# Performance work log

Measured on AMD Instinct MI355X. Metric: run time of the kernel, lower is better.

Reference implementation:

```python
import jax, jax.numpy as jnp
import numpy as np

D_MODEL = 1024
NUM_HEADS = 16
HEAD_DIM = D_MODEL // NUM_HEADS


def setup_inputs() -> dict:
    key = jax.random.key(0)
    ks = jax.random.split(key, 5)
    B, S = 2, 2048
    x = jax.random.normal(ks[0], (B, S, D_MODEL), dtype=jnp.float32)
    # nn.Linear(d,d,bias=False): y = x @ W.T, W is [out,in]. Init ~ U(-1/sqrt(d), 1/sqrt(d)).
    lim = 1.0 / np.sqrt(D_MODEL)
    wq = jax.random.uniform(ks[1], (D_MODEL, D_MODEL), jnp.float32, -lim, lim)
    wk = jax.random.uniform(ks[2], (D_MODEL, D_MODEL), jnp.float32, -lim, lim)
    wv = jax.random.uniform(ks[3], (D_MODEL, D_MODEL), jnp.float32, -lim, lim)
    wo = jax.random.uniform(ks[4], (D_MODEL, D_MODEL), jnp.float32, -lim, lim)
    return {"x": x, "wq": wq, "wk": wk, "wv": wv, "wo": wo}


def reference(x, wq, wk, wv, wo):
    B, S, D = x.shape
    H, Hd = NUM_HEADS, HEAD_DIM
    scale = Hd ** 0.5
    # projections (torch Linear: x @ W.T), split heads -> [B,H,S,Hd]
    q = (x @ wq.T).reshape(B, S, H, Hd).transpose(0, 2, 1, 3)
    k = (x @ wk.T).reshape(B, S, H, Hd).transpose(0, 2, 1, 3)
    v = (x @ wv.T).reshape(B, S, H, Hd).transpose(0, 2, 1, 3)
    scores = jnp.einsum('bhqd,bhkd->bhqk', q, k) / scale  # [B,H,S,S]
    # causal mask: disallow j > i
    causal_mask = jnp.triu(jnp.ones((S, S), dtype=bool), k=1)
    scores = jnp.where(causal_mask, -jnp.inf, scores)
    attn = jax.nn.softmax(scores, axis=-1)
    out = jnp.einsum('bhqk,bhkd->bhqd', attn, v)
    out = out.transpose(0, 2, 1, 3).reshape(B, S, D)
    return out @ wo.T
```

## Files before the change

kernel.cpp:

```cpp
#include <hip/hip_runtime.h>

#define DEV __device__ __forceinline__

typedef __attribute__((ext_vector_type(4))) float f32x4;
typedef __attribute__((ext_vector_type(8))) __bf16 bf16x8;

typedef __attribute__((address_space(1))) const uint32_t gu32;
typedef __attribute__((address_space(3))) uint32_t su32;

DEV void gload16(const void* g, void* s) {
  __builtin_amdgcn_global_load_lds((gu32*)(uintptr_t)g,
                                   (su32*)(uint32_t)(uintptr_t)s, 16, 0, 0);
}

DEV ushort bfbits(float f) { return __builtin_bit_cast(ushort, (__bf16)f); }

DEV bf16x8 lds8(const ushort* p) {
  return __builtin_bit_cast(bf16x8, *(const uint4*)(p));
}

DEV void vmcnt0bar() {
  asm volatile("s_waitcnt vmcnt(0)" ::: "memory");
  __builtin_amdgcn_s_barrier();
}

__global__ void cvt_all(const float* __restrict__ x, const float* __restrict__ wq,
                        const float* __restrict__ wk, const float* __restrict__ wv,
                        const float* __restrict__ wo, ushort* __restrict__ xb,
                        ushort* __restrict__ wb) {
  int i = blockIdx.x * blockDim.x + threadIdx.x;
  const float* src; ushort* dst; float scl = 1.0f; int j;
  if (i < 1048576) { src = x; dst = xb; j = i; }
  else {
    int t = (i - 1048576) >> 18;
    j = (i - 1048576) & 262143;
    src = t == 0 ? wq : (t == 1 ? wk : (t == 2 ? wv : wo));
    dst = wb + t * 1048576;
    if (t == 0) scl = 0.18033688011f;
  }
  float4 v = ((const float4*)src)[j];
  ushort4 o;
  o.x = bfbits(v.x * scl); o.y = bfbits(v.y * scl);
  o.z = bfbits(v.z * scl); o.w = bfbits(v.w * scl);
  ((ushort4*)dst)[j] = o;
}

template <int NFR, int OUT_MODE>
DEV void gemm_core(const ushort* __restrict__ A, const ushort* __restrict__ W,
                   void* __restrict__ Cout, ushort* sA, ushort* sB) {
  const int tid = threadIdx.x;
  const int l = tid & 63, wv = tid >> 6;
  const int g = l >> 4, lan = l & 15;
  const int wr = wv >> 1, wc = wv & 1;
  const int brow = blockIdx.y * 128, bcol = blockIdx.x * (NFR * 32);
  const int ASZ = 128 * 32, BSZ = NFR * 32 * 32;

  f32x4 acc[4][NFR] = {};

  auto stage = [&](int buf, int k0) {
    ushort* dA = sA + buf * ASZ;
    ushort* dB = sB + buf * BSZ;
#pragma unroll
    for (int i = 0; i < 2; ++i) {
      int n = i * 256 + wv * 64 + l;
      int row = n >> 2, ss = n & 3, gs = (ss - (row >> 1)) & 3;
      gload16(A + (size_t)(brow + row) * 1024 + k0 + gs * 8,
              dA + (i * 256 + wv * 64) * 8);
    }
#pragma unroll
    for (int i = 0; i < NFR / 2; ++i) {
      int n = i * 256 + wv * 64 + l;
      int row = n >> 2, ss = n & 3, gs = (ss - (row >> 1)) & 3;
      gload16(W + (size_t)(bcol + row) * 1024 + k0 + gs * 8,
              dB + (i * 256 + wv * 64) * 8);
    }
  };

  auto compute = [&](int buf) {
    const ushort* cA = sA + buf * ASZ;
    const ushort* cB = sB + buf * BSZ;
    bf16x8 a[4], b[NFR];
#pragma unroll
    for (int fr = 0; fr < 4; ++fr) {
      int row = wr * 64 + fr * 16 + lan;
      a[fr] = lds8(cA + row * 32 + 8 * (((row >> 1) + g) & 3));
    }
#pragma unroll
    for (int fn = 0; fn < NFR; ++fn) {
      int row = wc * (NFR * 16) + fn * 16 + lan;
      b[fn] = lds8(cB + row * 32 + 8 * (((row >> 1) + g) & 3));
    }
    __builtin_amdgcn_s_setprio(1);
#pragma unroll
    for (int fr = 0; fr < 4; ++fr)
#pragma unroll
      for (int fn = 0; fn < NFR; ++fn)
        acc[fr][fn] = __builtin_amdgcn_mfma_f32_16x16x32_bf16(a[fr], b[fn], acc[fr][fn], 0, 0, 0);
    __builtin_amdgcn_s_setprio(0);
  };

  stage(0, 0);
  vmcnt0bar();
#pragma unroll 1
  for (int t = 0; t < 15; ++t) {
    stage(1, (2 * t + 1) * 32); compute(0); vmcnt0bar();
    stage(0, (2 * t + 2) * 32); compute(1); vmcnt0bar();
  }
  stage(1, 31 * 32); compute(0); vmcnt0bar();
  compute(1);

#pragma unroll
  for (int fr = 0; fr < 4; ++fr)
#pragma unroll
    for (int fn = 0; fn < NFR; ++fn) {
      if (OUT_MODE == 2) {
        int row = brow + wr * 64 + fr * 16 + g * 4;
        int col = bcol + wc * (NFR * 16) + fn * 16 + lan;
        int bh2 = (row >> 11) * 16 + (col >> 6);
        int d = col & 63, s0 = row & 2047;
        ushort4 pk;
        pk.x = bfbits(acc[fr][fn][0]); pk.y = bfbits(acc[fr][fn][1]);
        pk.z = bfbits(acc[fr][fn][2]); pk.w = bfbits(acc[fr][fn][3]);
        *(ushort4*)((ushort*)Cout + ((size_t)bh2 * 64 + d) * 2048 + s0) = pk;
      } else {
#pragma unroll
        for (int r = 0; r < 4; ++r) {
          int row = brow + wr * 64 + fr * 16 + g * 4 + r;
          int col = bcol + wc * (NFR * 16) + fn * 16 + lan;
          if (OUT_MODE == 1)
            ((float*)Cout)[(size_t)row * 1024 + col] = acc[fr][fn][r];
          else
            ((ushort*)Cout)[(size_t)row * 1024 + col] = bfbits(acc[fr][fn][r]);
        }
      }
    }
}

__global__ __launch_bounds__(256) void gemm_qkv(
    const ushort* __restrict__ X, const ushort* __restrict__ Wb,
    ushort* __restrict__ Q, ushort* __restrict__ K, ushort* __restrict__ Vt) {
  __shared__ __align__(16) ushort sA[2 * 128 * 32];
  __shared__ __align__(16) ushort sB[2 * 128 * 32];
  const ushort* W = Wb + (size_t)blockIdx.z * 1048576;
  if (blockIdx.z == 2)
    gemm_core<4, 2>(X, W, (void*)Vt, sA, sB);
  else
    gemm_core<4, 0>(X, W, (void*)(blockIdx.z == 0 ? Q : K), sA, sB);
}

__global__ __launch_bounds__(256) void gemm_out(
    const ushort* __restrict__ AO, const ushort* __restrict__ Wo, float* __restrict__ C) {
  __shared__ __align__(16) ushort sA[2 * 128 * 32];
  __shared__ __align__(16) ushort sB[2 * 64 * 32];
  gemm_core<2, 1>(AO, Wo, (void*)C, sA, sB);
}

__global__ __launch_bounds__(256) void attn_fwd(
    const ushort* __restrict__ Qm, const ushort* __restrict__ Km,
    const ushort* __restrict__ Vtm, ushort* __restrict__ AO) {
  __shared__ __align__(16) ushort sK[2][64 * 64];
  __shared__ __align__(16) ushort sV[2][64 * 64];
  __shared__ __align__(16) ushort sP[4 * 16 * 64];

  const int tid = threadIdx.x;
  const int l = tid & 63, wv = tid >> 6;
  const int g = l >> 4, lan = l & 15;
  const int bid = blockIdx.x;
  const int j = bid >> 8, c = bid & 255;
  const int u = c >> 3, vv = c & 7;
  const int w = (u + ((j >> 1) << 4)) & 31;
  const int qt = (j & 1) ? (31 - w) : w;
  const int bh = vv + 8 * j;
  const int b = bh >> 4, h = bh & 15;
  const int q0 = qt * 64 + wv * 16;
  const int qg = q0 + lan;

  bf16x8 qf[2];
#pragma unroll
  for (int kf = 0; kf < 2; ++kf)
    qf[kf] = __builtin_bit_cast(bf16x8,
        *(const uint4*)(Qm + (size_t)(b * 2048 + qg) * 1024 + h * 64 + kf * 32 + g * 8));

  float lrun = 0.f;
  f32x4 o[4];
#pragma unroll
  for (int of = 0; of < 4; ++of) o[of] = (f32x4){0.f, 0.f, 0.f, 0.f};

  ushort* Pw = sP + wv * 1024;
  const int nkt = qt + 1;

  auto stagekv = [&](int buf, int kt) {
#pragma unroll
    for (int i = 0; i < 2; ++i) {
      int n = i * 256 + wv * 64 + l;
      int row = n >> 3, ss = n & 7, gs = ss ^ (row & 7);
      gload16(Km + (size_t)(b * 2048 + kt * 64 + row) * 1024 + h * 64 + gs * 8,
              sK[buf] + (i * 256 + wv * 64) * 8);
      gload16(Vtm + ((size_t)bh * 64 + row) * 2048 + kt * 64 + gs * 8,
              sV[buf] + (i * 256 + wv * 64) * 8);
    }
  };

  stagekv(0, 0);
  vmcnt0bar();

#pragma unroll 1
  for (int kt = 0; kt < nkt; ++kt) {
    const int buf = kt & 1;
    if (kt + 1 < nkt) stagekv(buf ^ 1, kt + 1);

    f32x4 sc[4];
    __builtin_amdgcn_s_setprio(1);
#pragma unroll
    for (int kvf = 0; kvf < 4; ++kvf) {
      f32x4 a2 = (f32x4){0.f, 0.f, 0.f, 0.f};
#pragma unroll
      for (int kf = 0; kf < 2; ++kf) {
        int row = kvf * 16 + lan;
        bf16x8 kb = lds8(sK[buf] + row * 64 + 8 * ((kf * 4 + g) ^ (row & 7)));
        a2 = __builtin_amdgcn_mfma_f32_16x16x32_bf16(kb, qf[kf], a2, 0, 0, 0);
      }
      sc[kvf] = a2;
    }
    __builtin_amdgcn_s_setprio(0);

    if (kt == qt) {
#pragma unroll
      for (int kvf = 0; kvf < 4; ++kvf)
#pragma unroll
        for (int r = 0; r < 4; ++r) {
          int kvg = kt * 64 + kvf * 16 + 4 * g + r;
          float p = __builtin_exp2f(sc[kvf][r]);
          p = (kvg <= qg) ? p : 0.f;
          sc[kvf][r] = p;
          lrun += p;
        }
    } else {
#pragma unroll
      for (int kvf = 0; kvf < 4; ++kvf)
#pragma unroll
        for (int r = 0; r < 4; ++r) {
          float p = __builtin_exp2f(sc[kvf][r]);
          sc[kvf][r] = p;
          lrun += p;
        }
    }

#pragma unroll
    for (int kvf = 0; kvf < 4; ++kvf) {
      ushort4 pk;
      pk.x = bfbits(sc[kvf][0]); pk.y = bfbits(sc[kvf][1]);
      pk.z = bfbits(sc[kvf][2]); pk.w = bfbits(sc[kvf][3]);
      *(ushort4*)(Pw + lan * 64 + ((16 * kvf + 4 * g) ^ ((lan & 7) << 3))) = pk;
    }
    bf16x8 pa[2];
#pragma unroll
    for (int kf = 0; kf < 2; ++kf)
      pa[kf] = lds8(Pw + lan * 64 + ((32 * kf + 8 * g) ^ ((lan & 7) << 3)));

    __builtin_amdgcn_s_setprio(1);
#pragma unroll
    for (int of = 0; of < 4; ++of)
#pragma unroll
      for (int kf = 0; kf < 2; ++kf) {
        int row = of * 16 + lan;
        bf16x8 vb = lds8(sV[buf] + row * 64 + 8 * ((kf * 4 + g) ^ (row & 7)));
        o[of] = __builtin_amdgcn_mfma_f32_16x16x32_bf16(pa[kf], vb, o[of], 0, 0, 0);
      }
    __builtin_amdgcn_s_setprio(0);

    vmcnt0bar();
  }

  lrun += __shfl_xor(lrun, 16);
  lrun += __shfl_xor(lrun, 32);
#pragma unroll
  for (int r = 0; r < 4; ++r) {
    float il = 1.0f / __shfl(lrun, g * 4 + r);
#pragma unroll
    for (int of = 0; of < 4; ++of) {
      int grow = q0 + g * 4 + r;
      AO[(size_t)(b * 2048 + grow) * 1024 + h * 64 + of * 16 + lan] = bfbits(o[of][r] * il);
    }
  }
}

extern "C" void kernel_launch(void* const* d_in, const int* in_sizes, int n_in,
                              void* d_out, int out_size, void* d_ws, size_t ws_size,
                              hipStream_t stream) {
  const float* x  = (const float*)d_in[0];
  const float* wq = (const float*)d_in[1];
  const float* wk = (const float*)d_in[2];
  const float* wv = (const float*)d_in[3];
  const float* wo = (const float*)d_in[4];
  float* out = (float*)d_out;

  char* ws = (char*)d_ws;
  const size_t MB = 1ull << 20;
  ushort* xb = (ushort*)(ws + 0);
  ushort* wb = (ushort*)(ws + 8 * MB);
  ushort* Q  = (ushort*)(ws + 16 * MB);
  ushort* K  = (ushort*)(ws + 24 * MB);
  ushort* Vt = (ushort*)(ws + 32 * MB);
  ushort* AO = (ushort*)(ws + 40 * MB);
  ushort* wob = wb + 3 * 1048576;

  cvt_all<<<8192, 256, 0, stream>>>(x, wq, wk, wv, wo, xb, wb);
  gemm_qkv<<<dim3(8, 32, 3), 256, 0, stream>>>(xb, wb, Q, K, Vt);
  attn_fwd<<<1024, 256, 0, stream>>>(Q, K, Vt, AO);
  gemm_out<<<dim3(16, 32), 256, 0, stream>>>(AO, wob, out);
}
```

Measured before the change: 181.5 us.

## Double attention query tile to 128 rows, reusing K/V fragments across two Q fragments

Each attention block now handles 128 query rows instead of 64, and each wave handles two 16-row query fragments. Every K and V fragment read from LDS feeds two MFMAs, and each staged K/V tile serves twice as many queries, which cuts LDS and global K/V traffic per unit of work. The grid shrinks to 512 blocks and the causal block pairing is remapped to match. In exchange the diagonal region now covers two masked tiles per block, register use rises, and there are fewer blocks to spread across the CUs.

```diff
diff --git a/kernel.cpp b/kernel.cpp
--- a/kernel.cpp
+++ b/kernel.cpp
@@ -160,34 +160,38 @@
     const ushort* __restrict__ Vtm, ushort* __restrict__ AO) {
   __shared__ __align__(16) ushort sK[2][64 * 64];
   __shared__ __align__(16) ushort sV[2][64 * 64];
-  __shared__ __align__(16) ushort sP[4 * 16 * 64];
+  __shared__ __align__(16) ushort sP[4 * 32 * 64];
 
   const int tid = threadIdx.x;
   const int l = tid & 63, wv = tid >> 6;
   const int g = l >> 4, lan = l & 15;
   const int bid = blockIdx.x;
   const int j = bid >> 8, c = bid & 255;
-  const int u = c >> 3, vv = c & 7;
-  const int w = (u + ((j >> 1) << 4)) & 31;
-  const int qt = (j & 1) ? (31 - w) : w;
-  const int bh = vv + 8 * j;
+  const int vv = c & 7, u = c >> 3;
+  const int w = u & 15, hi = u >> 4;
+  const int qt = j ? (15 - w) : w;
+  const int bh = vv + 8 * (2 * j + hi);
   const int b = bh >> 4, h = bh & 15;
-  const int q0 = qt * 64 + wv * 16;
-  const int qg = q0 + lan;
-
-  bf16x8 qf[2];
-#pragma unroll
-  for (int kf = 0; kf < 2; ++kf)
-    qf[kf] = __builtin_bit_cast(bf16x8,
-        *(const uint4*)(Qm + (size_t)(b * 2048 + qg) * 1024 + h * 64 + kf * 32 + g * 8));
-
-  float lrun = 0.f;
-  f32x4 o[4];
-#pragma unroll
-  for (int of = 0; of < 4; ++of) o[of] = (f32x4){0.f, 0.f, 0.f, 0.f};
-
-  ushort* Pw = sP + wv * 1024;
-  const int nkt = qt + 1;
+  const int q0 = qt * 128 + wv * 32;
+  const int nkt = 2 * qt + 2;
+
+  bf16x8 qf[2][2];
+#pragma unroll
+  for (int qfr = 0; qfr < 2; ++qfr)
+#pragma unroll
+    for (int kf = 0; kf < 2; ++kf)
+      qf[qfr][kf] = __builtin_bit_cast(bf16x8,
+          *(const uint4*)(Qm + (size_t)(b * 2048 + q0 + qfr * 16 + lan) * 1024 +
+                          h * 64 + kf * 32 + g * 8));
+
+  float lrun[2] = {0.f, 0.f};
+  f32x4 o[4][2];
+#pragma unroll
+  for (int of = 0; of < 4; ++of)
+#pragma unroll
+    for (int qfr = 0; qfr < 2; ++qfr) o[of][qfr] = (f32x4){0.f, 0.f, 0.f, 0.f};
+
+  ushort* Pw = sP + wv * 2048;
 
   auto stagekv = [&](int buf, int kt) {
 #pragma unroll
@@ -209,80 +213,104 @@
     const int buf = kt & 1;
     if (kt + 1 < nkt) stagekv(buf ^ 1, kt + 1);
 
-    f32x4 sc[4];
+    f32x4 sc[4][2];
     __builtin_amdgcn_s_setprio(1);
 #pragma unroll
     for (int kvf = 0; kvf < 4; ++kvf) {
-      f32x4 a2 = (f32x4){0.f, 0.f, 0.f, 0.f};
-#pragma unroll
-      for (int kf = 0; kf < 2; ++kf) {
-        int row = kvf * 16 + lan;
-        bf16x8 kb = lds8(sK[buf] + row * 64 + 8 * ((kf * 4 + g) ^ (row & 7)));
-        a2 = __builtin_amdgcn_mfma_f32_16x16x32_bf16(kb, qf[kf], a2, 0, 0, 0);
-      }
-      sc[kvf] = a2;
+      int row = kvf * 16 + lan;
+      bf16x8 kb0 = lds8(sK[buf] + row * 64 + 8 * ((0 * 4 + g) ^ (row & 7)));
+      bf16x8 kb1 = lds8(sK[buf] + row * 64 + 8 * ((1 * 4 + g) ^ (row & 7)));
+#pragma unroll
+      for (int qfr = 0; qfr < 2; ++qfr) {
+        f32x4 a2 = (f32x4){0.f, 0.f, 0.f, 0.f};
+        a2 = __builtin_amdgcn_mfma_f32_16x16x32_bf16(kb0, qf[qfr][0], a2, 0, 0, 0);
+        a2 = __builtin_amdgcn_mfma_f32_16x16x32_bf16(kb1, qf[qfr][1], a2, 0, 0, 0);
+        sc[kvf][qfr] = a2;
+      }
     }
     __builtin_amdgcn_s_setprio(0);
 
-    if (kt == qt) {
-#pragma unroll
-      for (int kvf = 0; kvf < 4; ++kvf)
-#pragma unroll
-        for (int r = 0; r < 4; ++r) {
-          int kvg = kt * 64 + kvf * 16 + 4 * g + r;
-          float p = __builtin_exp2f(sc[kvf][r]);
-          p = (kvg <= qg) ? p : 0.f;
-          sc[kvf][r] = p;
-          lrun += p;
-        }
+    if (kt >= 2 * qt) {
+#pragma unroll
+      for (int qfr = 0; qfr < 2; ++qfr) {
+        int qg = q0 + qfr * 16 + lan;
+#pragma unroll
+        for (int kvf = 0; kvf < 4; ++kvf)
+#pragma unroll
+          for (int r = 0; r < 4; ++r) {
+            int kvg = kt * 64 + kvf * 16 + 4 * g + r;
+            float p = __builtin_exp2f(sc[kvf][qfr][r]);
+            p = (kvg <= qg) ? p : 0.f;
+            sc[kvf][qfr][r] = p;
+            lrun[qfr] += p;
+          }
+      }
     } else {
 #pragma unroll
-      for (int kvf = 0; kvf < 4; ++kvf)
-#pragma unroll
-        for (int r = 0; r < 4; ++r) {
-          float p = __builtin_exp2f(sc[kvf][r]);
-          sc[kvf][r] = p;
-          lrun += p;
-        }
-    }
-
-#pragma unroll
-    for (int kvf = 0; kvf < 4; ++kvf) {
-      ushort4 pk;
-      pk.x = bfbits(sc[kvf][0]); pk.y = bfbits(sc[kvf][1]);
-      pk.z = bfbits(sc[kvf][2]); pk.w = bfbits(sc[kvf][3]);
-      *(ushort4*)(Pw + lan * 64 + ((16 * kvf + 4 * g) ^ ((lan & 7) << 3))) = pk;
-    }
-    bf16x8 pa[2];
-#pragma unroll
-    for (int kf = 0; kf < 2; ++kf)
-      pa[kf] = lds8(Pw + lan * 64 + ((32 * kf + 8 * g) ^ ((lan & 7) << 3)));
+      for (int qfr = 0; qfr < 2; ++qfr)
+#pragma unroll
+        for (int kvf = 0; kvf < 4; ++kvf)
+#pragma unroll
+          for (int r = 0; r < 4; ++r) {
+            float p = __builtin_exp2f(sc[kvf][qfr][r]);
+            sc[kvf][qfr][r] = p;
+            lrun[qfr] += p;
+          }
+    }
+
+#pragma unroll
+    for (int qfr = 0; qfr < 2; ++qfr) {
+      int prow = qfr * 16 + lan;
+#pragma unroll
+      for (int kvf = 0; kvf < 4; ++kvf) {
+        ushort4 pk;
+        pk.x = bfbits(sc[kvf][qfr][0]); pk.y = bfbits(sc[kvf][qfr][1]);
+        pk.z = bfbits(sc[kvf][qfr][2]); pk.w = bfbits(sc[kvf][qfr][3]);
+        *(ushort4*)(Pw + prow * 64 + ((16 * kvf + 4 * g) ^ ((prow & 7) << 3))) = pk;
+      }
+    }
+    bf16x8 pa[2][2];
+#pragma unroll
+    for (int qfr = 0; qfr < 2; ++qfr) {
+      int prow = qfr * 16 + lan;
+#pragma unroll
+      for (int kf = 0; kf < 2; ++kf)
+        pa[qfr][kf] = lds8(Pw + prow * 64 + ((32 * kf + 8 * g) ^ ((prow & 7) << 3)));
+    }
 
     __builtin_amdgcn_s_setprio(1);
 #pragma unroll
-    for (int of = 0; of < 4; ++of)
-#pragma unroll
-      for (int kf = 0; kf < 2; ++kf) {
-        int row = of * 16 + lan;
-        bf16x8 vb = lds8(sV[buf] + row * 64 + 8 * ((kf * 4 + g) ^ (row & 7)));
-        o[of] = __builtin_amdgcn_mfma_f32_16x16x32_bf16(pa[kf], vb, o[of], 0, 0, 0);
-      }
+    for (int of = 0; of < 4; ++of) {
+      int row = of * 16 + lan;
+      bf16x8 vb0 = lds8(sV[buf] + row * 64 + 8 * ((0 * 4 + g) ^ (row & 7)));
+      bf16x8 vb1 = lds8(sV[buf] + row * 64 + 8 * ((1 * 4 + g) ^ (row & 7)));
+#pragma unroll
+      for (int qfr = 0; qfr < 2; ++qfr) {
+        o[of][qfr] = __builtin_amdgcn_mfma_f32_16x16x32_bf16(pa[qfr][0], vb0, o[of][qfr], 0, 0, 0);
+        o[of][qfr] = __builtin_amdgcn_mfma_f32_16x16x32_bf16(pa[qfr][1], vb1, o[of][qfr], 0, 0, 0);
+      }
+    }
     __builtin_amdgcn_s_setprio(0);
 
     vmcnt0bar();
   }
 
-  lrun += __shfl_xor(lrun, 16);
-  lrun += __shfl_xor(lrun, 32);
-#pragma unroll
-  for (int r = 0; r < 4; ++r) {
-    float il = 1.0f / __shfl(lrun, g * 4 + r);
-#pragma unroll
-    for (int of = 0; of < 4; ++of) {
-      int grow = q0 + g * 4 + r;
-      AO[(size_t)(b * 2048 + grow) * 1024 + h * 64 + of * 16 + lan] = bfbits(o[of][r] * il);
-    }
+#pragma unroll
+  for (int qfr = 0; qfr < 2; ++qfr) {
+    lrun[qfr] += __shfl_xor(lrun[qfr], 16);
+    lrun[qfr] += __shfl_xor(lrun[qfr], 32);
   }
+#pragma unroll
+  for (int qfr = 0; qfr < 2; ++qfr)
+#pragma unroll
+    for (int r = 0; r < 4; ++r) {
+      float il = 1.0f / __shfl(lrun[qfr], g * 4 + r);
+      int grow = q0 + qfr * 16 + g * 4 + r;
+#pragma unroll
+      for (int of = 0; of < 4; ++of)
+        AO[(size_t)(b * 2048 + grow) * 1024 + h * 64 + of * 16 + lan] =
+            bfbits(o[of][qfr][r] * il);
+    }
 }
 
 extern "C" void kernel_launch(void* const* d_in, const int* in_sizes, int n_in,
@@ -307,6 +335,6 @@
 
   cvt_all<<<8192, 256, 0, stream>>>(x, wq, wk, wv, wo, xb, wb);
   gemm_qkv<<<dim3(8, 32, 3), 256, 0, stream>>>(xb, wb, Q, K, Vt);
-  attn_fwd<<<1024, 256, 0, stream>>>(Q, K, Vt, AO);
+  attn_fwd<<<512, 256, 0, stream>>>(Q, K, Vt, AO);
   gemm_out<<<dim3(16, 32), 256, 0, stream>>>(AO, wob, out);
 }
```

Result: faster. 176.8 us (-2.6%).

## Make attention kernel persistent with atomic work queue, longest-first ordering

Applied to the files above, without the earlier changes.

Replaces the fixed one-tile-per-block attention launch with 768 persistent blocks that pull (query tile, batch-head) jobs from a global atomic counter. Jobs are issued longest-first (largest causal query tile first) to reduce tail imbalance. When the workspace is too small it falls back to a static two-job schedule. It adds a memset launch, an atomic plus a block barrier per job, and loses the previous L2-friendly interleaving of heads.

```diff
diff --git a/kernel.cpp b/kernel.cpp
--- a/kernel.cpp
+++ b/kernel.cpp
@@ -155,132 +155,149 @@
   gemm_core<2, 1>(AO, Wo, (void*)C, sA, sB);
 }
 
+#define NJOBS 1024
 __global__ __launch_bounds__(256) void attn_fwd(
     const ushort* __restrict__ Qm, const ushort* __restrict__ Km,
-    const ushort* __restrict__ Vtm, ushort* __restrict__ AO) {
+    const ushort* __restrict__ Vtm, ushort* __restrict__ AO,
+    uint* __restrict__ cnt) {
   __shared__ __align__(16) ushort sK[2][64 * 64];
   __shared__ __align__(16) ushort sV[2][64 * 64];
   __shared__ __align__(16) ushort sP[4 * 16 * 64];
+  __shared__ uint jobid_s;
 
   const int tid = threadIdx.x;
   const int l = tid & 63, wv = tid >> 6;
   const int g = l >> 4, lan = l & 15;
-  const int bid = blockIdx.x;
-  const int j = bid >> 8, c = bid & 255;
-  const int u = c >> 3, vv = c & 7;
-  const int w = (u + ((j >> 1) << 4)) & 31;
-  const int qt = (j & 1) ? (31 - w) : w;
-  const int bh = vv + 8 * j;
-  const int b = bh >> 4, h = bh & 15;
-  const int q0 = qt * 64 + wv * 16;
-  const int qg = q0 + lan;
-
-  bf16x8 qf[2];
-#pragma unroll
-  for (int kf = 0; kf < 2; ++kf)
-    qf[kf] = __builtin_bit_cast(bf16x8,
-        *(const uint4*)(Qm + (size_t)(b * 2048 + qg) * 1024 + h * 64 + kf * 32 + g * 8));
-
-  float lrun = 0.f;
-  f32x4 o[4];
-#pragma unroll
-  for (int of = 0; of < 4; ++of) o[of] = (f32x4){0.f, 0.f, 0.f, 0.f};
-
   ushort* Pw = sP + wv * 1024;
-  const int nkt = qt + 1;
-
-  auto stagekv = [&](int buf, int kt) {
-#pragma unroll
-    for (int i = 0; i < 2; ++i) {
-      int n = i * 256 + wv * 64 + l;
-      int row = n >> 3, ss = n & 7, gs = ss ^ (row & 7);
-      gload16(Km + (size_t)(b * 2048 + kt * 64 + row) * 1024 + h * 64 + gs * 8,
-              sK[buf] + (i * 256 + wv * 64) * 8);
-      gload16(Vtm + ((size_t)bh * 64 + row) * 2048 + kt * 64 + gs * 8,
-              sV[buf] + (i * 256 + wv * 64) * 8);
-    }
-  };
-
-  stagekv(0, 0);
-  vmcnt0bar();
-
+
+  int grab = 0;
 #pragma unroll 1
-  for (int kt = 0; kt < nkt; ++kt) {
-    const int buf = kt & 1;
-    if (kt + 1 < nkt) stagekv(buf ^ 1, kt + 1);
-
-    f32x4 sc[4];
-    __builtin_amdgcn_s_setprio(1);
-#pragma unroll
-    for (int kvf = 0; kvf < 4; ++kvf) {
-      f32x4 a2 = (f32x4){0.f, 0.f, 0.f, 0.f};
-#pragma unroll
-      for (int kf = 0; kf < 2; ++kf) {
-        int row = kvf * 16 + lan;
-        bf16x8 kb = lds8(sK[buf] + row * 64 + 8 * ((kf * 4 + g) ^ (row & 7)));
-        a2 = __builtin_amdgcn_mfma_f32_16x16x32_bf16(kb, qf[kf], a2, 0, 0, 0);
-      }
-      sc[kvf] = a2;
-    }
-    __builtin_amdgcn_s_setprio(0);
-
-    if (kt == qt) {
-#pragma unroll
-      for (int kvf = 0; kvf < 4; ++kvf)
-#pragma unroll
-        for (int r = 0; r < 4; ++r) {
-          int kvg = kt * 64 + kvf * 16 + 4 * g + r;
-          float p = __builtin_exp2f(sc[kvf][r]);
-          p = (kvg <= qg) ? p : 0.f;
-          sc[kvf][r] = p;
-          lrun += p;
+  for (;;) {
+    uint job;
+    if (cnt) {
+      if (tid == 0) jobid_s = atomicAdd(cnt, 1u);
+      __syncthreads();
+      job = jobid_s;
+      if (job >= NJOBS) break;
+    } else {
+      if (grab == 0) job = blockIdx.x;
+      else if (grab == 1 && (int)blockIdx.x < NJOBS - (int)gridDim.x)
+        job = NJOBS - 1 - blockIdx.x;
+      else break;
+      ++grab;
+    }
+
+    const int qt = 31 - (int)(job >> 5);
+    const int bh = (int)(job & 31);
+    const int b = bh >> 4, h = bh & 15;
+    const int q0 = qt * 64 + wv * 16;
+    const int qg = q0 + lan;
+    const int nkt = qt + 1;
+
+    bf16x8 qf[2];
+#pragma unroll
+    for (int kf = 0; kf < 2; ++kf)
+      qf[kf] = __builtin_bit_cast(bf16x8,
+          *(const uint4*)(Qm + (size_t)(b * 2048 + qg) * 1024 + h * 64 + kf * 32 + g * 8));
+
+    float lrun = 0.f;
+    f32x4 o[4];
+#pragma unroll
+    for (int of = 0; of < 4; ++of) o[of] = (f32x4){0.f, 0.f, 0.f, 0.f};
+
+    auto stagekv = [&](int buf, int kt) {
+#pragma unroll
+      for (int i = 0; i < 2; ++i) {
+        int n = i * 256 + wv * 64 + l;
+        int row = n >> 3, ss = n & 7, gs = ss ^ (row & 7);
+        gload16(Km + (size_t)(b * 2048 + kt * 64 + row) * 1024 + h * 64 + gs * 8,
+                sK[buf] + (i * 256 + wv * 64) * 8);
+        gload16(Vtm + ((size_t)bh * 64 + row) * 2048 + kt * 64 + gs * 8,
+                sV[buf] + (i * 256 + wv * 64) * 8);
+      }
+    };
+
+    stagekv(0, 0);
+    vmcnt0bar();
+
+#pragma unroll 1
+    for (int kt = 0; kt < nkt; ++kt) {
+      const int buf = kt & 1;
+      if (kt + 1 < nkt) stagekv(buf ^ 1, kt + 1);
+
+      f32x4 sc[4];
+      __builtin_amdgcn_s_setprio(1);
+#pragma unroll
+      for (int kvf = 0; kvf < 4; ++kvf) {
+        f32x4 a2 = (f32x4){0.f, 0.f, 0.f, 0.f};
+#pragma unroll
+        for (int kf = 0; kf < 2; ++kf) {
+          int row = kvf * 16 + lan;
+          bf16x8 kb = lds8(sK[buf] + row * 64 + 8 * ((kf * 4 + g) ^ (row & 7)));
+          a2 = __builtin_amdgcn_mfma_f32_16x16x32_bf16(kb, qf[kf], a2, 0, 0, 0);
         }
-    } else {
-#pragma unroll
-      for (int kvf = 0; kvf < 4; ++kvf)
-#pragma unroll
-        for (int r = 0; r < 4; ++r) {
-          float p = __builtin_exp2f(sc[kvf][r]);
-          sc[kvf][r] = p;
-          lrun += p;
+        sc[kvf] = a2;
+      }
+      __builtin_amdgcn_s_setprio(0);
+
+      if (kt == qt) {
+#pragma unroll
+        for (int kvf = 0; kvf < 4; ++kvf)
+#pragma unroll
+          for (int r = 0; r < 4; ++r) {
+            int kvg = kt * 64 + kvf * 16 + 4 * g + r;
+            float p = __builtin_exp2f(sc[kvf][r]);
+            p = (kvg <= qg) ? p : 0.f;
+            sc[kvf][r] = p;
+            lrun += p;
+          }
+      } else {
+#pragma unroll
+        for (int kvf = 0; kvf < 4; ++kvf)
+#pragma unroll
+          for (int r = 0; r < 4; ++r) {
+            float p = __builtin_exp2f(sc[kvf][r]);
+            sc[kvf][r] = p;
+            lrun += p;
+          }
+      }
+
+#pragma unroll
+      for (int kvf = 0; kvf < 4; ++kvf) {
+        ushort4 pk;
+        pk.x = bfbits(sc[kvf][0]); pk.y = bfbits(sc[kvf][1]);
+        pk.z = bfbits(sc[kvf][2]); pk.w = bfbits(sc[kvf][3]);
+        *(ushort4*)(Pw + lan * 64 + ((16 * kvf + 4 * g) ^ ((lan & 7) << 3))) = pk;
+      }
+      bf16x8 pa[2];
+#pragma unroll
+      for (int kf = 0; kf < 2; ++kf)
+        pa[kf] = lds8(Pw + lan * 64 + ((32 * kf + 8 * g) ^ ((lan & 7) << 3)));
+
+      __builtin_amdgcn_s_setprio(1);
+#pragma unroll
+      for (int of = 0; of < 4; ++of)
+#pragma unroll
+        for (int kf = 0; kf < 2; ++kf) {
+          int row = of * 16 + lan;
+          bf16x8 vb = lds8(sV[buf] + row * 64 + 8 * ((kf * 4 + g) ^ (row & 7)));
+          o[of] = __builtin_amdgcn_mfma_f32_16x16x32_bf16(pa[kf], vb, o[of], 0, 0, 0);
         }
-    }
-
-#pragma unroll
-    for (int kvf = 0; kvf < 4; ++kvf) {
-      ushort4 pk;
-      pk.x = bfbits(sc[kvf][0]); pk.y = bfbits(sc[kvf][1]);
-      pk.z = bfbits(sc[kvf][2]); pk.w = bfbits(sc[kvf][3]);
-      *(ushort4*)(Pw + lan * 64 + ((16 * kvf + 4 * g) ^ ((lan & 7) << 3))) = pk;
-    }
-    bf16x8 pa[2];
-#pragma unroll
-    for (int kf = 0; kf < 2; ++kf)
-      pa[kf] = lds8(Pw + lan * 64 + ((32 * kf + 8 * g) ^ ((lan & 7) << 3)));
-
-    __builtin_amdgcn_s_setprio(1);
-#pragma unroll
-    for (int of = 0; of < 4; ++of)
-#pragma unroll
-      for (int kf = 0; kf < 2; ++kf) {
-        int row = of * 16 + lan;
-        bf16x8 vb = lds8(sV[buf] + row * 64 + 8 * ((kf * 4 + g) ^ (row & 7)));
-        o[of] = __builtin_amdgcn_mfma_f32_16x16x32_bf16(pa[kf], vb, o[of], 0, 0, 0);
-      }
-    __builtin_amdgcn_s_setprio(0);
-
-    vmcnt0bar();
-  }
-
-  lrun += __shfl_xor(lrun, 16);
-  lrun += __shfl_xor(lrun, 32);
-#pragma unroll
-  for (int r = 0; r < 4; ++r) {
-    float il = 1.0f / __shfl(lrun, g * 4 + r);
-#pragma unroll
-    for (int of = 0; of < 4; ++of) {
-      int grow = q0 + g * 4 + r;
-      AO[(size_t)(b * 2048 + grow) * 1024 + h * 64 + of * 16 + lan] = bfbits(o[of][r] * il);
+      __builtin_amdgcn_s_setprio(0);
+
+      vmcnt0bar();
+    }
+
+    lrun += __shfl_xor(lrun, 16);
+    lrun += __shfl_xor(lrun, 32);
+#pragma unroll
+    for (int r = 0; r < 4; ++r) {
+      float il = 1.0f / __shfl(lrun, g * 4 + r);
+#pragma unroll
+      for (int of = 0; of < 4; ++of) {
+        int grow = q0 + g * 4 + r;
+        AO[(size_t)(b * 2048 + grow) * 1024 + h * 64 + of * 16 + lan] = bfbits(o[of][r] * il);
+      }
     }
   }
 }
@@ -305,8 +322,14 @@
   ushort* AO = (ushort*)(ws + 40 * MB);
   ushort* wob = wb + 3 * 1048576;
 
+  uint* cnt = nullptr;
+  if (ws_size >= 49 * MB) {
+    cnt = (uint*)(ws + ws_size - 256);
+    hipMemsetAsync(cnt, 0, 4, stream);
+  }
+
   cvt_all<<<8192, 256, 0, stream>>>(x, wq, wk, wv, wo, xb, wb);
   gemm_qkv<<<dim3(8, 32, 3), 256, 0, stream>>>(xb, wb, Q, K, Vt);
-  attn_fwd<<<1024, 256, 0, stream>>>(Q, K, Vt, AO);
+  attn_fwd<<<768, 256, 0, stream>>>(Q, K, Vt, AO, cnt);
   gemm_out<<<dim3(16, 32), 256, 0, stream>>>(AO, wob, out);
 }
```

Result: no change. 183.0 us (+0.8%).
